# Performance work log

Measured on AMD Instinct MI355X. Metric: run time of the kernel, lower is better.

## Reference

```python
import jax, jax.numpy as jnp
import numpy as np

# dims
B, N, D = 4, 1024, 768
H, HD = 12, 64            # num_heads, head_dim (routed q heads = top-H experts)
EA = 24                   # num_attn_experts
EF, KF = 8, 2             # num_ffd_experts, ffd_heads (top-k for FFN MoE)
HS = int(4 * D) // KF     # ffn expert head_size = 1536
T = 9                     # task_num
S = 1                     # shared FFN experts: max(1, int(8*0.1))


def layernorm(x, g, b, eps=1e-5):
    m = x.mean(-1, keepdims=True)
    v = ((x - m) ** 2).mean(-1, keepdims=True)
    return (x - m) * jax.lax.rsqrt(v + eps) * g + b


def setup_inputs() -> dict:
    key = jax.random.key(0)
    ks = jax.random.split(key, 16)
    s = 0.02
    rn = lambda k, shp: jax.random.normal(k, shp, dtype=jnp.float32)
    return {
        "x": rn(ks[0], (B, N, D)),
        "task_bh": 3,
        "ln1_g": jnp.ones((D,), jnp.float32), "ln1_b": jnp.zeros((D,), jnp.float32),
        "ln2_g": jnp.ones((D,), jnp.float32), "ln2_b": jnp.zeros((D,), jnp.float32),
        "gate_a": rn(ks[1], (T, D, EA)) * s,
        "Wq_in": rn(ks[2], (EA, D, HD)) * s,
        "Wq_out": rn(ks[3], (EA, HD, D)) * s,
        "W_kv": rn(ks[4], (D, 2 * HD)) * s, "b_kv": jnp.zeros((2 * HD,), jnp.float32),
        "gate_f": rn(ks[5], (T, D, EF)) * s,
        "W1f": rn(ks[6], (EF, D, HS)) * s, "b1f": jnp.zeros((EF, HS), jnp.float32),
        "W2f": rn(ks[7], (EF, HS, D)) * s, "b_out": jnp.zeros((D,), jnp.float32),
        "Ws1": rn(ks[8], (S, D, HS)) * s, "bs1": jnp.zeros((S, HS), jnp.float32),
        "Ws2": rn(ks[9], (S, HS, D)) * s,
    }


def _route(h, gate_w, k):
    # h: [B,N,D], gate_w: [D,E] -> normalized top-k weights + one-hot dispatch
    probs = jax.nn.softmax(jnp.einsum("bnd,de->bne", h, gate_w), axis=-1)
    topv, topi = jax.lax.top_k(probs, k)                 # [B,N,k]
    topv = topv / topv.sum(-1, keepdims=True)
    oh = jax.nn.one_hot(topi, probs.shape[-1], dtype=h.dtype)  # [B,N,k,E]
    return topv, oh


def reference(x, task_bh, ln1_g, ln1_b, ln2_g, ln2_b, gate_a, Wq_in, Wq_out,
              W_kv, b_kv, gate_f, W1f, b1f, W2f, b_out, Ws1, bs1, Ws2):
    # --- MoE attention (routed q heads, shared single-head k/v) ---
    h = layernorm(x, ln1_g, ln1_b)
    topv, oh = _route(h, gate_a[task_bh], H)             # [B,N,H], [B,N,H,EA]
    h_all = jnp.einsum("bnd,edh->bneh", h, Wq_in)        # all-expert q projections
    q = jnp.einsum("bnke,bneh->bnkh", oh, h_all)         # gathered q heads [B,N,H,HD]
    kv = h @ W_kv + b_kv
    kk, vv = kv[..., :HD], kv[..., HD:]                  # [B,N,HD]
    att = jnp.einsum("bihd,bjd->bhij", q, kk) * (HD ** -0.5)
    att = jax.nn.softmax(att, axis=-1)
    o = jnp.einsum("bhij,bjd->bihd", att, vv)            # [B,N,H,HD]
    dense = jnp.einsum("bnk,bnke,bnkh->bneh", topv, oh, o)  # scatter to experts
    y = jnp.einsum("bneh,ehd->bnd", dense, Wq_out)       # gated expert output proj
    x = x + y

    # --- MoE FFN (top-KF routed experts + shared experts) ---
    h = layernorm(x, ln2_g, ln2_b)
    topv, oh = _route(h, gate_f[task_bh], KF)            # [B,N,KF], [B,N,KF,EF]
    h_all = jax.nn.gelu(jnp.einsum("bnd,edh->bneh", h, W1f) + b1f, approximate=False)
    wdense = jnp.einsum("bnk,bnke->bne", topv, oh)       # per-expert gate weights
    y = jnp.einsum("bne,bneh,ehd->bnd", wdense, h_all, W2f) + b_out
    hs = jax.nn.gelu(jnp.einsum("bnd,sdh->bnsh", h, Ws1) + bs1, approximate=False)
    y = y + jnp.einsum("bnsh,shd->bnd", hs, Ws2)         # always-on shared experts
    return x + y
```

## Files before the change

kernel.cpp:

```cpp
#include <hip/hip_runtime.h>
#include <hip/hip_bf16.h>

#define NTOK 4096
#define DDIM 768
#define NEA  24
#define NHEAD 12
#define HDIM 64
#define NEF  8
#define HSD  1536
#define SEQL 1024
#define NB   4
#define MAXTILE 104
#define NQKV 1664

using bf16 = __hip_bfloat16;

typedef float v4f __attribute__((ext_vector_type(4)));
typedef short v8s __attribute__((ext_vector_type(8)));
typedef __bf16 v8bf __attribute__((ext_vector_type(8)));

typedef __attribute__((address_space(3))) unsigned lds_u32_t;
typedef const __attribute__((address_space(1))) unsigned glb_u32_t;

__device__ __forceinline__ void gload16(const void* g, void* l) {
  __builtin_amdgcn_global_load_lds((glb_u32_t*)g, (lds_u32_t*)l, 16, 0, 0);
}

__device__ __forceinline__ float gelu_f(float x) {
  return 0.5f * x * (1.0f + erff(x * 0.70710678118654752440f));
}

__device__ __forceinline__ short f2bf_s(float x) {
  bf16 h = __float2bfloat16(x);
  return __builtin_bit_cast(short, h);
}

__device__ __forceinline__ int xcd_swz(int lin, int nwg) {
  return (lin & 7) * (nwg >> 3) + (lin >> 3);
}

__device__ __forceinline__ void gemm_core(const short* gA0, const short* gA1,
                                          const short* gB0, const short* gB1,
                                          short* lA, short* lB, int steps,
                                          v4f (&acc)[4][4])
{
  const int tid = threadIdx.x;
  const int w = tid >> 6, l = tid & 63;
  const int wr = (w >> 1) * 64, wc = (w & 1) * 64;
  const int fr = l & 15, ko = (l >> 4) * 8;
  const int sb = w * 1024;
  gload16(gA0, lA + sb); gload16(gA1, lA + sb + 512);
  gload16(gB0, lB + sb); gload16(gB1, lB + sb + 512);
  gA0 += 32; gA1 += 32; gB0 += 32; gB1 += 32;
  __syncthreads();
  int cur = 0;
  for (int s = 0; s < steps; ++s) {
    const int nxt = cur ^ 1;
    if (s + 1 < steps) {
      gload16(gA0, lA + nxt * 4096 + sb);
      gload16(gA1, lA + nxt * 4096 + sb + 512);
      gload16(gB0, lB + nxt * 4096 + sb);
      gload16(gB1, lB + nxt * 4096 + sb + 512);
      gA0 += 32; gA1 += 32; gB0 += 32; gB1 += 32;
    }
    const short* bA = lA + cur * 4096;
    const short* bB = lB + cur * 4096;
    v8s av[4], bv[4];
#pragma unroll
    for (int mi = 0; mi < 4; ++mi)
      av[mi] = *(const v8s*)(bA + (wr + mi * 16 + fr) * 32 + ko);
#pragma unroll
    for (int ni = 0; ni < 4; ++ni)
      bv[ni] = *(const v8s*)(bB + (wc + ni * 16 + fr) * 32 + ko);
#pragma unroll
    for (int mi = 0; mi < 4; ++mi)
#pragma unroll
      for (int ni = 0; ni < 4; ++ni)
        acc[mi][ni] = __builtin_amdgcn_mfma_f32_16x16x32_bf16(
            __builtin_bit_cast(v8bf, av[mi]), __builtin_bit_cast(v8bf, bv[ni]),
            acc[mi][ni], 0, 0, 0);
    __syncthreads();
    cur = nxt;
  }
}

template<int EPI>
__global__ __launch_bounds__(256, 4) void k_gemm(const short* __restrict__ A,
    const short* __restrict__ Bt, float* __restrict__ C, bf16* __restrict__ Cb,
    const float* __restrict__ addsrc, int N, int K)
{
  const int nwg = gridDim.x * gridDim.y;
  const int swz = xcd_swz(blockIdx.x + gridDim.x * blockIdx.y, nwg);
  const int m0 = (swz % gridDim.x) * 128, n0 = (swz / gridDim.x) * 128;
  __shared__ __align__(16) short lA[2 * 128 * 32];
  __shared__ __align__(16) short lB[2 * 128 * 32];
  const int tid = threadIdx.x, w = tid >> 6, l = tid & 63;
  const int ca = w * 128 + l, cb = ca + 64;
  const short* gA0 = A + (size_t)(m0 + (ca >> 2)) * K + (ca & 3) * 8;
  const short* gA1 = A + (size_t)(m0 + (cb >> 2)) * K + (cb & 3) * 8;
  const short* gB0 = Bt + (size_t)(n0 + (ca >> 2)) * K + (ca & 3) * 8;
  const short* gB1 = Bt + (size_t)(n0 + (cb >> 2)) * K + (cb & 3) * 8;
  v4f acc[4][4];
  v4f z = {0.f, 0.f, 0.f, 0.f};
#pragma unroll
  for (int i = 0; i < 4; ++i)
#pragma unroll
    for (int j = 0; j < 4; ++j) acc[i][j] = z;
  gemm_core(gA0, gA1, gB0, gB1, lA, lB, K >> 5, acc);
  const int wr = (w >> 1) * 64, wc = (w & 1) * 64;
  const int fr = l & 15, rq = (l >> 4) * 4;
#pragma unroll
  for (int mi = 0; mi < 4; ++mi)
#pragma unroll
    for (int ni = 0; ni < 4; ++ni)
#pragma unroll
      for (int j = 0; j < 4; ++j) {
        int rg = m0 + wr + mi * 16 + rq + j;
        int cg = n0 + wc + ni * 16 + fr;
        float v = acc[mi][ni][j];
        if (EPI == 2) v += addsrc[(size_t)rg * N + cg];
        if (EPI == 3) Cb[(size_t)rg * N + cg] = __float2bfloat16(v);
        else          C[(size_t)rg * N + cg] = v;
      }
}

template<int PHASE>
__global__ __launch_bounds__(256, 5) void k_gemm_moe(
    const short* __restrict__ Aact, const short* __restrict__ Wt,
    const short* __restrict__ Wst, const float* __restrict__ b1f,
    const float* __restrict__ bs1, const float* __restrict__ wsl,
    const int* __restrict__ off, const int* __restrict__ cnt,
    const int* __restrict__ list, const int* __restrict__ tmeta,
    const int* __restrict__ ntl, short* __restrict__ outb,
    float* __restrict__ outf)
{
  constexpr int K = (PHASE == 0) ? DDIM : HSD;
  constexpr int N = (PHASE == 0) ? HSD : DDIM;
  const int nwg = gridDim.x * gridDim.y;
  const int swz = xcd_swz(blockIdx.x + gridDim.x * blockIdx.y, nwg);
  const int ti = swz % gridDim.x;
  const int n0 = (swz / gridDim.x) * 128;
  if (ti >= ntl[0]) return;
  const int mm = tmeta[ti];
  const int e = mm >> 20;
  const int r0 = mm & 0xFFFFF;
  const int base = (e < 8) ? off[e] : NTOK * 2;
  const int c    = (e < 8) ? cnt[e] : NTOK;
  const int rows = c - r0;
  const short* Bt = (e < 8) ? Wt + (size_t)e * N * K : Wst;
  __shared__ __align__(16) short lA[2 * 128 * 32];
  __shared__ __align__(16) short lB[2 * 128 * 32];
  const int tid = threadIdx.x, w = tid >> 6, l = tid & 63;
  const int ca = w * 128 + l, cb = ca + 64;

  auto arowptr = [&](int chunk) -> const short* {
    int r = chunk >> 2;
    int re = (r < rows) ? r : (rows - 1);
    int slot = base + r0 + re;
    if (PHASE == 0) {
      int tok = (e < 8) ? list[slot] : (slot - NTOK * 2);
      return Aact + (size_t)tok * DDIM;
    } else {
      return Aact + (size_t)slot * HSD;
    }
  };
  const short* gA0 = arowptr(ca) + (ca & 3) * 8;
  const short* gA1 = arowptr(cb) + (cb & 3) * 8;
  const short* gB0 = Bt + (size_t)(n0 + (ca >> 2)) * K + (ca & 3) * 8;
  const short* gB1 = Bt + (size_t)(n0 + (cb >> 2)) * K + (cb & 3) * 8;
  v4f acc[4][4];
  v4f z = {0.f, 0.f, 0.f, 0.f};
#pragma unroll
  for (int i = 0; i < 4; ++i)
#pragma unroll
    for (int j = 0; j < 4; ++j) acc[i][j] = z;
  gemm_core(gA0, gA1, gB0, gB1, lA, lB, K >> 5, acc);
  const int wr = (w >> 1) * 64, wc = (w & 1) * 64;
  const int fr = l & 15, rq = (l >> 4) * 4;
  const float* bias = (PHASE == 0) ? ((e < 8) ? b1f + e * HSD : bs1) : nullptr;
#pragma unroll
  for (int mi = 0; mi < 4; ++mi)
#pragma unroll
    for (int ni = 0; ni < 4; ++ni)
#pragma unroll
      for (int j = 0; j < 4; ++j) {
        int rl = wr + mi * 16 + rq + j;
        if (rl >= rows) continue;
        int slot = base + r0 + rl;
        int cg = n0 + wc + ni * 16 + fr;
        float v = acc[mi][ni][j];
        if (PHASE == 0) {
          v = gelu_f(v + bias[cg]);
          outb[(size_t)slot * HSD + cg] = f2bf_s(v);
        } else {
          outf[(size_t)slot * DDIM + cg] = v * wsl[slot];
        }
      }
}

__global__ __launch_bounds__(256) void k_lnrouteA(const float* __restrict__ x,
    const float* __restrict__ lg_, const float* __restrict__ lb_,
    const float* __restrict__ gt, bf16* __restrict__ hb,
    int* __restrict__ topi, float* __restrict__ topv)
{
  const int t = blockIdx.x * 4 + (threadIdx.x >> 6);
  const int l = threadIdx.x & 63;
  const float* xr = x + (size_t)t * DDIM;
  float v[12];
  float s = 0.f, q = 0.f;
#pragma unroll
  for (int m = 0; m < 12; ++m) {
    v[m] = xr[l + 64 * m];
    s += v[m]; q += v[m] * v[m];
  }
#pragma unroll
  for (int m = 32; m >= 1; m >>= 1) { s += __shfl_xor(s, m); q += __shfl_xor(q, m); }
  const float mean = s * (1.f / DDIM);
  const float inv = rsqrtf(q * (1.f / DDIM) - mean * mean + 1e-5f);
  float hr[12];
#pragma unroll
  for (int m = 0; m < 12; ++m) {
    int d = l + 64 * m;
    hr[m] = (v[m] - mean) * inv * lg_[d] + lb_[d];
    hb[(size_t)t * DDIM + d] = __float2bfloat16(hr[m]);
  }
  float lg[NEA];
#pragma unroll
  for (int e = 0; e < NEA; ++e) {
    const float* ge = gt + e * DDIM;
    float a = 0.f;
#pragma unroll
    for (int m = 0; m < 12; ++m) a += hr[m] * ge[l + 64 * m];
#pragma unroll
    for (int m = 32; m >= 1; m >>= 1) a += __shfl_xor(a, m);
    lg[e] = a;
  }
  unsigned used = 0;
  int sel[NHEAD]; float bvk[NHEAD];
#pragma unroll
  for (int k = 0; k < NHEAD; ++k) {
    float bv = -3e30f; int best = 0;
#pragma unroll
    for (int e = 0; e < NEA; ++e)
      if (!((used >> e) & 1u) && lg[e] > bv) { bv = lg[e]; best = e; }
    used |= 1u << best; sel[k] = best; bvk[k] = bv;
  }
  const float mx = bvk[0];
  float pvk[NHEAD], ssum = 0.f;
#pragma unroll
  for (int k = 0; k < NHEAD; ++k) { pvk[k] = expf(bvk[k] - mx); ssum += pvk[k]; }
  const float invs = 1.f / ssum;
  if (l == 0) {
#pragma unroll
    for (int k = 0; k < NHEAD; ++k) {
      topi[t * NHEAD + k] = sel[k];
      topv[t * NHEAD + k] = pvk[k] * invs;
    }
  }
}

__global__ __launch_bounds__(256) void k_lnrouteF(const float* __restrict__ x,
    const float* __restrict__ lg_, const float* __restrict__ lb_,
    const float* __restrict__ gt, bf16* __restrict__ hb,
    int* __restrict__ ef, float* __restrict__ wf, int* __restrict__ cnt)
{
  const int t = blockIdx.x * 4 + (threadIdx.x >> 6);
  const int l = threadIdx.x & 63;
  const float* xr = x + (size_t)t * DDIM;
  float v[12];
  float s = 0.f, q = 0.f;
#pragma unroll
  for (int m = 0; m < 12; ++m) {
    v[m] = xr[l + 64 * m];
    s += v[m]; q += v[m] * v[m];
  }
#pragma unroll
  for (int m = 32; m >= 1; m >>= 1) { s += __shfl_xor(s, m); q += __shfl_xor(q, m); }
  const float mean = s * (1.f / DDIM);
  const float inv = rsqrtf(q * (1.f / DDIM) - mean * mean + 1e-5f);
  float hr[12];
#pragma unroll
  for (int m = 0; m < 12; ++m) {
    int d = l + 64 * m;
    hr[m] = (v[m] - mean) * inv * lg_[d] + lb_[d];
    hb[(size_t)t * DDIM + d] = __float2bfloat16(hr[m]);
  }
  float lg[NEF];
#pragma unroll
  for (int e = 0; e < NEF; ++e) {
    const float* ge = gt + e * DDIM;
    float a = 0.f;
#pragma unroll
    for (int m = 0; m < 12; ++m) a += hr[m] * ge[l + 64 * m];
#pragma unroll
    for (int m = 32; m >= 1; m >>= 1) a += __shfl_xor(a, m);
    lg[e] = a;
  }
  unsigned used = 0;
  int sel[2]; float bvk[2];
#pragma unroll
  for (int k = 0; k < 2; ++k) {
    float bv = -3e30f; int best = 0;
#pragma unroll
    for (int e = 0; e < NEF; ++e)
      if (!((used >> e) & 1u) && lg[e] > bv) { bv = lg[e]; best = e; }
    used |= 1u << best; sel[k] = best; bvk[k] = bv;
  }
  const float mx = bvk[0];
  float p0 = expf(bvk[0] - mx), p1 = expf(bvk[1] - mx);
  const float invs = 1.f / (p0 + p1);
  if (l == 0) {
    ef[t * 2 + 0] = sel[0]; wf[t * 2 + 0] = p0 * invs;
    ef[t * 2 + 1] = sel[1]; wf[t * 2 + 1] = p1 * invs;
    atomicAdd(&cnt[sel[0]], 1);
    atomicAdd(&cnt[sel[1]], 1);
  }
}

__global__ void k_packGT(const float* __restrict__ src, const int* __restrict__ task,
                         float* __restrict__ dst, int E)
{
  int idx = blockIdx.x * 256 + threadIdx.x;
  if (idx >= E * DDIM) return;
  int e = idx / DDIM, d = idx - e * DDIM;
  dst[idx] = src[(size_t)task[0] * DDIM * E + (size_t)d * E + e];
}

__global__ void k_off(const int* __restrict__ cnt, int* __restrict__ off,
                      int* __restrict__ cur, int* __restrict__ tmeta,
                      int* __restrict__ ntl)
{
  if (threadIdx.x == 0 && blockIdx.x == 0) {
    int a = 0;
    for (int e = 0; e < NEF; ++e) { off[e] = a; cur[e] = a; a += cnt[e]; }
    off[NEF] = a;
    int n = 0;
    for (int e = 0; e < NEF; ++e)
      for (int r = 0; r < cnt[e]; r += 128) tmeta[n++] = (e << 20) | r;
    for (int r = 0; r < NTOK; r += 128) tmeta[n++] = (8 << 20) | r;
    ntl[0] = n;
  }
}

__global__ void k_fill(const int* __restrict__ ef, const float* __restrict__ wf,
                       int* __restrict__ cur, int* __restrict__ list,
                       float* __restrict__ wsl, int* __restrict__ sof)
{
  int t = blockIdx.x * 256 + threadIdx.x;
  if (t >= NTOK) return;
  for (int k = 0; k < 2; ++k) {
    int e = ef[t * 2 + k];
    int slot = atomicAdd(&cur[e], 1);
    list[slot] = t;
    wsl[slot] = wf[t * 2 + k];
    sof[t * 2 + k] = slot;
  }
  list[NTOK * 2 + t] = t;
  wsl[NTOK * 2 + t] = 1.f;
}

__global__ void k_packKV(const bf16* __restrict__ hq, const float* __restrict__ bkv,
                         bf16* __restrict__ kvb)
{
  int idx = blockIdx.x * 256 + threadIdx.x;
  int t = idx >> 7, j = idx & 127;
  float v = __bfloat162float(hq[(size_t)t * NQKV + 1536 + j]) + bkv[j];
  kvb[idx] = __float2bfloat16(v);
}

__global__ void k_scatter(const float* __restrict__ o, const int* __restrict__ topi,
                          const float* __restrict__ topv, bf16* __restrict__ dense)
{
  int idx = blockIdx.x * 256 + threadIdx.x;
  int t = idx / (NHEAD * HDIM);
  int rem = idx - t * (NHEAD * HDIM);
  int k = rem >> 6, hd = rem & 63;
  float v = topv[t * NHEAD + k] * o[idx];
  dense[(size_t)t * (NEA * HDIM) + topi[t * NHEAD + k] * HDIM + hd] = __float2bfloat16(v);
}

__global__ __launch_bounds__(256, 2) void k_attn_mfma(const bf16* __restrict__ hq,
    const int* __restrict__ topi, const bf16* __restrict__ kv, float* __restrict__ o)
{
  __shared__ __align__(16) short Qs[64 * 64];
  __shared__ __align__(16) short Ks[64 * 64];
  __shared__ __align__(16) short Vs[64 * 64];
  __shared__ __align__(16) short Ps[64 * 64];
  const int i0 = blockIdx.x * 64;
  const int h = blockIdx.y;
  const int b = blockIdx.z;
  const int tid = threadIdx.x;
  const int w = tid >> 6, l = tid & 63;
  const int g = l >> 4, fq = l & 15;
  const short* qg = (const short*)hq;
  const short* kvg = (const short*)kv;

  {
    int c0 = tid, c1 = tid + 256;
    int r0 = c0 >> 3, s0 = (c0 & 7) ^ (r0 & 7);
    int r1 = c1 >> 3, s1 = (c1 & 7) ^ (r1 & 7);
    int t0 = b * SEQL + i0 + r0, t1 = b * SEQL + i0 + r1;
    int e0 = topi[t0 * NHEAD + h], e1 = topi[t1 * NHEAD + h];
    gload16(qg + (size_t)t0 * NQKV + e0 * HDIM + s0 * 8, Qs + w * 512);
    gload16(qg + (size_t)t1 * NQKV + e1 * HDIM + s1 * 8, Qs + 2048 + w * 512);
  }

  float m_run[4], l_run[4];
  v4f oacc[4];
#pragma unroll
  for (int r = 0; r < 4; ++r) { m_run[r] = -1e30f; l_run[r] = 0.f; }
#pragma unroll
  for (int nd = 0; nd < 4; ++nd) oacc[nd] = (v4f){0.f, 0.f, 0.f, 0.f};

  const int vj = tid & 63;
  const int vd0 = (tid >> 6) * 16;

  for (int jt = 0; jt < 16; ++jt) {
    if (jt) __syncthreads();
    {
      int c0 = tid, c1 = tid + 256;
      int r0 = c0 >> 3, s0 = (c0 & 7) ^ (r0 & 7);
      int r1 = c1 >> 3, s1 = (c1 & 7) ^ (r1 & 7);
      gload16(kvg + ((size_t)(b * SEQL + jt * 64 + r0)) * 128 + s0 * 8,
              Ks + w * 512);
      gload16(kvg + ((size_t)(b * SEQL + jt * 64 + r1)) * 128 + s1 * 8,
              Ks + 2048 + w * 512);
    }
    {
      const short* gv = kvg + ((size_t)(b * SEQL + jt * 64 + vj)) * 128 + 64 + vd0;
      v8s a0 = *(const v8s*)gv;
      v8s a1 = *(const v8s*)(gv + 8);
#pragma unroll
      for (int k2 = 0; k2 < 8; ++k2) {
        int d = vd0 + k2;
        Vs[d * 64 + (((vj >> 3) ^ (d & 7)) << 3) + (vj & 7)] = a0[k2];
      }
#pragma unroll
      for (int k2 = 0; k2 < 8; ++k2) {
        int d = vd0 + 8 + k2;
        Vs[d * 64 + (((vj >> 3) ^ (d & 7)) << 3) + (vj & 7)] = a1[k2];
      }
    }
    __syncthreads();

    v8s aq[2];
#pragma unroll
    for (int kk = 0; kk < 2; ++kk)
      aq[kk] = *(const v8s*)&Qs[(16 * w + fq) * 64 + (((kk * 4 + g) ^ (fq & 7)) << 3)];
    v4f sacc[4];
#pragma unroll
    for (int n = 0; n < 4; ++n) {
      sacc[n] = (v4f){0.f, 0.f, 0.f, 0.f};
#pragma unroll
      for (int kk = 0; kk < 2; ++kk) {
        v8s bk = *(const v8s*)&Ks[(16 * n + fq) * 64 + (((kk * 4 + g) ^ (fq & 7)) << 3)];
        sacc[n] = __builtin_amdgcn_mfma_f32_16x16x32_bf16(
            __builtin_bit_cast(v8bf, aq[kk]), __builtin_bit_cast(v8bf, bk),
            sacc[n], 0, 0, 0);
      }
    }
#pragma unroll
    for (int n = 0; n < 4; ++n) sacc[n] *= 0.125f;

#pragma unroll
    for (int r = 0; r < 4; ++r) {
      float mt = fmaxf(fmaxf(sacc[0][r], sacc[1][r]), fmaxf(sacc[2][r], sacc[3][r]));
      mt = fmaxf(mt, __shfl_xor(mt, 1));
      mt = fmaxf(mt, __shfl_xor(mt, 2));
      mt = fmaxf(mt, __shfl_xor(mt, 4));
      mt = fmaxf(mt, __shfl_xor(mt, 8));
      float mnew = fmaxf(m_run[r], mt);
      float corr = __expf(m_run[r] - mnew);
      float pv[4], ps = 0.f;
#pragma unroll
      for (int n = 0; n < 4; ++n) { pv[n] = __expf(sacc[n][r] - mnew); ps += pv[n]; }
      ps += __shfl_xor(ps, 1);
      ps += __shfl_xor(ps, 2);
      ps += __shfl_xor(ps, 4);
      ps += __shfl_xor(ps, 8);
      l_run[r] = l_run[r] * corr + ps;
      m_run[r] = mnew;
#pragma unroll
      for (int nd = 0; nd < 4; ++nd) oacc[nd][r] *= corr;
      int qrow = 16 * w + 4 * g + r;
#pragma unroll
      for (int n = 0; n < 4; ++n)
        Ps[qrow * 64 + (((2 * n + (fq >> 3)) ^ (qrow & 7)) << 3) + (fq & 7)] =
            f2bf_s(pv[n]);
    }
    asm volatile("s_waitcnt lgkmcnt(0)" ::: "memory");
    __builtin_amdgcn_sched_barrier(0);

#pragma unroll
    for (int kk = 0; kk < 2; ++kk) {
      v8s pa = *(const v8s*)&Ps[(16 * w + fq) * 64 + (((kk * 4 + g) ^ (fq & 7)) << 3)];
#pragma unroll
      for (int nd = 0; nd < 4; ++nd) {
        v8s vb = *(const v8s*)&Vs[(16 * nd + fq) * 64 + (((kk * 4 + g) ^ (fq & 7)) << 3)];
        oacc[nd] = __builtin_amdgcn_mfma_f32_16x16x32_bf16(
            __builtin_bit_cast(v8bf, pa), __builtin_bit_cast(v8bf, vb),
            oacc[nd], 0, 0, 0);
      }
    }
  }

#pragma unroll
  for (int r = 0; r < 4; ++r) {
    float inv = 1.f / l_run[r];
    int qgl = i0 + 16 * w + 4 * g + r;
#pragma unroll
    for (int nd = 0; nd < 4; ++nd)
      o[(((size_t)b * SEQL + qgl) * NHEAD + h) * HDIM + 16 * nd + fq] =
          oacc[nd][r] * inv;
  }
}

__global__ __launch_bounds__(256) void k_packT(const float* __restrict__ src,
                                               bf16* __restrict__ dst, int K, int N)
{
  __shared__ float tile[32][33];
  const size_t zoff = (size_t)blockIdx.z * K * N;
  const int k0 = blockIdx.x * 32, n0 = blockIdx.y * 32;
  const int tx = threadIdx.x & 31, ty = threadIdx.x >> 5;
#pragma unroll
  for (int i = 0; i < 32; i += 8)
    tile[ty + i][tx] = src[zoff + (size_t)(k0 + ty + i) * N + n0 + tx];
  __syncthreads();
#pragma unroll
  for (int i = 0; i < 32; i += 8)
    dst[zoff + (size_t)(n0 + ty + i) * K + k0 + tx] =
        __float2bfloat16(tile[tx][ty + i]);
}

__global__ void k_final(const float* __restrict__ x2, const float* __restrict__ bout,
                        const float* __restrict__ yp, const int* __restrict__ sof,
                        float* __restrict__ out)
{
  int idx = blockIdx.x * 256 + threadIdx.x;
  int t = idx / DDIM, d = idx - t * DDIM;
  int s0 = sof[2 * t], s1 = sof[2 * t + 1];
  out[idx] = x2[idx] + bout[d] + yp[(size_t)s0 * DDIM + d] + yp[(size_t)s1 * DDIM + d] +
             yp[((size_t)(NTOK * 2) + t) * DDIM + d];
}

extern "C" void kernel_launch(void* const* d_in, const int* in_sizes, int n_in,
                              void* d_out, int out_size, void* d_ws, size_t ws_size,
                              hipStream_t stream) {
  const float* x      = (const float*)d_in[0];
  const int*   task   = (const int*)d_in[1];
  const float* ln1g   = (const float*)d_in[2];
  const float* ln1b   = (const float*)d_in[3];
  const float* ln2g   = (const float*)d_in[4];
  const float* ln2b   = (const float*)d_in[5];
  const float* gate_a = (const float*)d_in[6];
  const float* wq_in  = (const float*)d_in[7];
  const float* wq_out = (const float*)d_in[8];
  const float* w_kv   = (const float*)d_in[9];
  const float* b_kv   = (const float*)d_in[10];
  const float* gate_f = (const float*)d_in[11];
  const float* w1f    = (const float*)d_in[12];
  const float* b1f    = (const float*)d_in[13];
  const float* w2f    = (const float*)d_in[14];
  const float* b_out  = (const float*)d_in[15];
  const float* ws1    = (const float*)d_in[16];
  const float* bs1    = (const float*)d_in[17];
  const float* ws2    = (const float*)d_in[18];

  char* W = (char*)d_ws;
  size_t off_ = 0;
  auto alloc = [&](size_t b) { size_t o = off_; off_ += (b + 255) & ~(size_t)255; return o; };
  size_t o_reg1  = alloc(37748736);
  size_t o_h1b   = o_reg1;
  size_t o_hallq = o_reg1 + 6291456;
  size_t o_hmid  = o_reg1;
  size_t o_q     = alloc(12582912);
  size_t o_o     = alloc(12582912);
  size_t o_dense = alloc(12582912);
  size_t o_ypart = o_q;
  size_t o_kvb   = alloc(1048576);
  size_t o_x2    = alloc(12582912);
  size_t o_h2b   = alloc(6291456);
  size_t o_btq   = alloc(2555904);
  size_t o_wqot  = alloc(2359296);
  size_t o_w1t   = alloc(18874368);
  size_t o_w2t   = alloc(18874368);
  size_t o_ws1t  = alloc(2359296);
  size_t o_ws2t  = alloc(2359296);
  size_t o_topi  = alloc(196608);
  size_t o_topv  = alloc(196608);
  size_t o_ef    = alloc(32768);
  size_t o_wf    = alloc(32768);
  size_t o_cnt   = alloc(1024);
  size_t o_offs  = alloc(1024);
  size_t o_cur   = alloc(1024);
  size_t o_list  = alloc(49152);
  size_t o_wsl   = alloc(49152);
  size_t o_sof   = alloc(32768);
  size_t o_tmeta = alloc(1024);
  size_t o_ntl   = alloc(256);
  size_t o_gta   = alloc(73728);
  size_t o_gtf   = alloc(24576);
  if (ws_size < off_) return;

  bf16*  h1b   = (bf16*)(W + o_h1b);
  bf16*  hallqb= (bf16*)(W + o_hallq);
  float* ob    = (float*)(W + o_o);
  bf16*  dense = (bf16*)(W + o_dense);
  bf16*  kvbb  = (bf16*)(W + o_kvb);
  float* x2b   = (float*)(W + o_x2);
  bf16*  h2b   = (bf16*)(W + o_h2b);
  short* hmid  = (short*)(W + o_hmid);
  float* ypart = (float*)(W + o_ypart);
  int*   topi  = (int*)(W + o_topi);
  float* topv  = (float*)(W + o_topv);
  int*   efp   = (int*)(W + o_ef);
  float* wfp   = (float*)(W + o_wf);
  int*   cntp  = (int*)(W + o_cnt);
  int*   offp  = (int*)(W + o_offs);
  int*   curp  = (int*)(W + o_cur);
  int*   listp = (int*)(W + o_list);
  float* wslp  = (float*)(W + o_wsl);
  int*   sofp  = (int*)(W + o_sof);
  int*   tmeta = (int*)(W + o_tmeta);
  int*   ntl   = (int*)(W + o_ntl);
  float* gta   = (float*)(W + o_gta);
  float* gtf   = (float*)(W + o_gtf);

  k_packT<<<dim3(24, 2, 24), 256, 0, stream>>>(wq_in, (bf16*)(W + o_btq), 768, 64);
  k_packT<<<dim3(24, 4, 1), 256, 0, stream>>>(w_kv, (bf16*)(W + o_btq) + 1536 * 768, 768, 128);
  k_packT<<<dim3(48, 24, 1), 256, 0, stream>>>(wq_out, (bf16*)(W + o_wqot), 1536, 768);
  k_packT<<<dim3(24, 48, 8), 256, 0, stream>>>(w1f, (bf16*)(W + o_w1t), 768, 1536);
  k_packT<<<dim3(48, 24, 8), 256, 0, stream>>>(w2f, (bf16*)(W + o_w2t), 1536, 768);
  k_packT<<<dim3(24, 48, 1), 256, 0, stream>>>(ws1, (bf16*)(W + o_ws1t), 768, 1536);
  k_packT<<<dim3(48, 24, 1), 256, 0, stream>>>(ws2, (bf16*)(W + o_ws2t), 1536, 768);
  k_packGT<<<dim3(72), 256, 0, stream>>>(gate_a, task, gta, NEA);
  k_packGT<<<dim3(24), 256, 0, stream>>>(gate_f, task, gtf, NEF);

  (void)hipMemsetAsync(W + o_dense, 0, 12582912, stream);
  (void)hipMemsetAsync(W + o_cnt, 0, 64, stream);

  k_lnrouteA<<<NTOK / 4, 256, 0, stream>>>(x, ln1g, ln1b, gta, h1b, topi, topv);

  k_gemm<3><<<dim3(32, 13), 256, 0, stream>>>((const short*)h1b, (const short*)(W + o_btq),
                                              nullptr, hallqb, nullptr, NQKV, 768);

  k_packKV<<<dim3(2048), 256, 0, stream>>>(hallqb, b_kv, kvbb);
  k_attn_mfma<<<dim3(16, NHEAD, NB), 256, 0, stream>>>(hallqb, topi, kvbb, ob);
  k_scatter<<<dim3(12288), 256, 0, stream>>>(ob, topi, topv, dense);

  k_gemm<2><<<dim3(32, 6), 256, 0, stream>>>((const short*)dense, (const short*)(W + o_wqot),
                                             x2b, nullptr, x, 768, 1536);

  k_lnrouteF<<<NTOK / 4, 256, 0, stream>>>(x2b, ln2g, ln2b, gtf, h2b, efp, wfp, cntp);
  k_off<<<1, 1, 0, stream>>>(cntp, offp, curp, tmeta, ntl);
  k_fill<<<16, 256, 0, stream>>>(efp, wfp, curp, listp, wslp, sofp);

  k_gemm_moe<0><<<dim3(MAXTILE, 12), 256, 0, stream>>>((const short*)h2b,
      (const short*)(W + o_w1t), (const short*)(W + o_ws1t), b1f, bs1, nullptr,
      offp, cntp, listp, tmeta, ntl, hmid, nullptr);
  k_gemm_moe<1><<<dim3(MAXTILE, 6), 256, 0, stream>>>((const short*)hmid,
      (const short*)(W + o_w2t), (const short*)(W + o_ws2t), nullptr, nullptr, wslp,
      offp, cntp, listp, tmeta, ntl, nullptr, ypart);

  k_final<<<dim3(12288), 256, 0, stream>>>(x2b, b_out, ypart, sofp, (float*)d_out);
}
```

Baseline: 532.4 us.

## Fuse attention scatter into epilogue, split-K output proj, atomic MoE accumulation

The gated scatter to expert slots moves into the attention epilogue, so the separate scatter kernel and the fp32 attention-output buffer go away. The attention output projection now uses split-K (2 slices) with atomicAdd into a residual buffer prefilled by a device copy of x. The FFN second-phase GEMM atomically accumulates weighted expert outputs per token, so the final kernel no longer gathers slot partials. This trades extra memset/memcpy traffic and atomic contention for fewer kernels and less intermediate memory, and makes the floating-point summation order nondeterministic.

```diff
diff --git a/kernel.cpp b/kernel.cpp
--- a/kernel.cpp
+++ b/kernel.cpp
@@ -87,26 +87,28 @@
 template<int EPI>
 __global__ __launch_bounds__(256, 4) void k_gemm(const short* __restrict__ A,
     const short* __restrict__ Bt, float* __restrict__ C, bf16* __restrict__ Cb,
-    const float* __restrict__ addsrc, int N, int K)
+    int N, int K)
 {
   const int nwg = gridDim.x * gridDim.y;
   const int swz = xcd_swz(blockIdx.x + gridDim.x * blockIdx.y, nwg);
   const int m0 = (swz % gridDim.x) * 128, n0 = (swz / gridDim.x) * 128;
+  const int kspl = (EPI == 4) ? (K / (int)gridDim.z) : K;
+  const int kbase = (EPI == 4) ? (int)blockIdx.z * kspl : 0;
   __shared__ __align__(16) short lA[2 * 128 * 32];
   __shared__ __align__(16) short lB[2 * 128 * 32];
   const int tid = threadIdx.x, w = tid >> 6, l = tid & 63;
   const int ca = w * 128 + l, cb = ca + 64;
-  const short* gA0 = A + (size_t)(m0 + (ca >> 2)) * K + (ca & 3) * 8;
-  const short* gA1 = A + (size_t)(m0 + (cb >> 2)) * K + (cb & 3) * 8;
-  const short* gB0 = Bt + (size_t)(n0 + (ca >> 2)) * K + (ca & 3) * 8;
-  const short* gB1 = Bt + (size_t)(n0 + (cb >> 2)) * K + (cb & 3) * 8;
+  const short* gA0 = A + (size_t)(m0 + (ca >> 2)) * K + (ca & 3) * 8 + kbase;
+  const short* gA1 = A + (size_t)(m0 + (cb >> 2)) * K + (cb & 3) * 8 + kbase;
+  const short* gB0 = Bt + (size_t)(n0 + (ca >> 2)) * K + (ca & 3) * 8 + kbase;
+  const short* gB1 = Bt + (size_t)(n0 + (cb >> 2)) * K + (cb & 3) * 8 + kbase;
   v4f acc[4][4];
   v4f z = {0.f, 0.f, 0.f, 0.f};
 #pragma unroll
   for (int i = 0; i < 4; ++i)
 #pragma unroll
     for (int j = 0; j < 4; ++j) acc[i][j] = z;
-  gemm_core(gA0, gA1, gB0, gB1, lA, lB, K >> 5, acc);
+  gemm_core(gA0, gA1, gB0, gB1, lA, lB, kspl >> 5, acc);
   const int wr = (w >> 1) * 64, wc = (w & 1) * 64;
   const int fr = l & 15, rq = (l >> 4) * 4;
 #pragma unroll
@@ -118,9 +120,9 @@
         int rg = m0 + wr + mi * 16 + rq + j;
         int cg = n0 + wc + ni * 16 + fr;
         float v = acc[mi][ni][j];
-        if (EPI == 2) v += addsrc[(size_t)rg * N + cg];
-        if (EPI == 3) Cb[(size_t)rg * N + cg] = __float2bfloat16(v);
-        else          C[(size_t)rg * N + cg] = v;
+        if (EPI == 3)      Cb[(size_t)rg * N + cg] = __float2bfloat16(v);
+        else if (EPI == 4) atomicAdd(&C[(size_t)rg * N + cg], v);
+        else               C[(size_t)rg * N + cg] = v;
       }
 }
 
@@ -193,7 +195,8 @@
           v = gelu_f(v + bias[cg]);
           outb[(size_t)slot * HSD + cg] = f2bf_s(v);
         } else {
-          outf[(size_t)slot * DDIM + cg] = v * wsl[slot];
+          int tok = (e < 8) ? list[slot] : (slot - NTOK * 2);
+          atomicAdd(&outf[(size_t)tok * DDIM + cg], v * wsl[slot]);
         }
       }
 }
@@ -344,7 +347,7 @@
 
 __global__ void k_fill(const int* __restrict__ ef, const float* __restrict__ wf,
                        int* __restrict__ cur, int* __restrict__ list,
-                       float* __restrict__ wsl, int* __restrict__ sof)
+                       float* __restrict__ wsl)
 {
   int t = blockIdx.x * 256 + threadIdx.x;
   if (t >= NTOK) return;
@@ -353,7 +356,6 @@
     int slot = atomicAdd(&cur[e], 1);
     list[slot] = t;
     wsl[slot] = wf[t * 2 + k];
-    sof[t * 2 + k] = slot;
   }
   list[NTOK * 2 + t] = t;
   wsl[NTOK * 2 + t] = 1.f;
@@ -368,19 +370,9 @@
   kvb[idx] = __float2bfloat16(v);
 }
 
-__global__ void k_scatter(const float* __restrict__ o, const int* __restrict__ topi,
-                          const float* __restrict__ topv, bf16* __restrict__ dense)
-{
-  int idx = blockIdx.x * 256 + threadIdx.x;
-  int t = idx / (NHEAD * HDIM);
-  int rem = idx - t * (NHEAD * HDIM);
-  int k = rem >> 6, hd = rem & 63;
-  float v = topv[t * NHEAD + k] * o[idx];
-  dense[(size_t)t * (NEA * HDIM) + topi[t * NHEAD + k] * HDIM + hd] = __float2bfloat16(v);
-}
-
 __global__ __launch_bounds__(256, 2) void k_attn_mfma(const bf16* __restrict__ hq,
-    const int* __restrict__ topi, const bf16* __restrict__ kv, float* __restrict__ o)
+    const int* __restrict__ topi, const float* __restrict__ topv,
+    const bf16* __restrict__ kv, bf16* __restrict__ dense)
 {
   __shared__ __align__(16) short Qs[64 * 64];
   __shared__ __align__(16) short Ks[64 * 64];
@@ -506,12 +498,13 @@
 
 #pragma unroll
   for (int r = 0; r < 4; ++r) {
-    float inv = 1.f / l_run[r];
-    int qgl = i0 + 16 * w + 4 * g + r;
+    int t = b * SEQL + i0 + 16 * w + 4 * g + r;
+    int e = topi[t * NHEAD + h];
+    float sc = topv[t * NHEAD + h] / l_run[r];
 #pragma unroll
     for (int nd = 0; nd < 4; ++nd)
-      o[(((size_t)b * SEQL + qgl) * NHEAD + h) * HDIM + 16 * nd + fq] =
-          oacc[nd][r] * inv;
+      dense[(size_t)t * (NEA * HDIM) + e * HDIM + 16 * nd + fq] =
+          __float2bfloat16(oacc[nd][r] * sc);
   }
 }
 
@@ -533,14 +526,11 @@
 }
 
 __global__ void k_final(const float* __restrict__ x2, const float* __restrict__ bout,
-                        const float* __restrict__ yp, const int* __restrict__ sof,
-                        float* __restrict__ out)
+                        const float* __restrict__ yacc, float* __restrict__ out)
 {
   int idx = blockIdx.x * 256 + threadIdx.x;
-  int t = idx / DDIM, d = idx - t * DDIM;
-  int s0 = sof[2 * t], s1 = sof[2 * t + 1];
-  out[idx] = x2[idx] + bout[d] + yp[(size_t)s0 * DDIM + d] + yp[(size_t)s1 * DDIM + d] +
-             yp[((size_t)(NTOK * 2) + t) * DDIM + d];
+  int d = idx % DDIM;
+  out[idx] = x2[idx] + bout[d] + yacc[idx];
 }
 
 extern "C" void kernel_launch(void* const* d_in, const int* in_sizes, int n_in,
@@ -573,10 +563,8 @@
   size_t o_h1b   = o_reg1;
   size_t o_hallq = o_reg1 + 6291456;
   size_t o_hmid  = o_reg1;
-  size_t o_q     = alloc(12582912);
-  size_t o_o     = alloc(12582912);
+  size_t o_yacc  = alloc(12582912);
   size_t o_dense = alloc(12582912);
-  size_t o_ypart = o_q;
   size_t o_kvb   = alloc(1048576);
   size_t o_x2    = alloc(12582912);
   size_t o_h2b   = alloc(6291456);
@@ -595,7 +583,6 @@
   size_t o_cur   = alloc(1024);
   size_t o_list  = alloc(49152);
   size_t o_wsl   = alloc(49152);
-  size_t o_sof   = alloc(32768);
   size_t o_tmeta = alloc(1024);
   size_t o_ntl   = alloc(256);
   size_t o_gta   = alloc(73728);
@@ -604,13 +591,12 @@
 
   bf16*  h1b   = (bf16*)(W + o_h1b);
   bf16*  hallqb= (bf16*)(W + o_hallq);
-  float* ob    = (float*)(W + o_o);
+  float* yacc  = (float*)(W + o_yacc);
   bf16*  dense = (bf16*)(W + o_dense);
   bf16*  kvbb  = (bf16*)(W + o_kvb);
   float* x2b   = (float*)(W + o_x2);
   bf16*  h2b   = (bf16*)(W + o_h2b);
   short* hmid  = (short*)(W + o_hmid);
-  float* ypart = (float*)(W + o_ypart);
   int*   topi  = (int*)(W + o_topi);
   float* topv  = (float*)(W + o_topv);
   int*   efp   = (int*)(W + o_ef);
@@ -620,7 +606,6 @@
   int*   curp  = (int*)(W + o_cur);
   int*   listp = (int*)(W + o_list);
   float* wslp  = (float*)(W + o_wsl);
-  int*   sofp  = (int*)(W + o_sof);
   int*   tmeta = (int*)(W + o_tmeta);
   int*   ntl   = (int*)(W + o_ntl);
   float* gta   = (float*)(W + o_gta);
@@ -638,29 +623,31 @@
 
   (void)hipMemsetAsync(W + o_dense, 0, 12582912, stream);
   (void)hipMemsetAsync(W + o_cnt, 0, 64, stream);
+  (void)hipMemsetAsync(W + o_yacc, 0, 12582912, stream);
 
   k_lnrouteA<<<NTOK / 4, 256, 0, stream>>>(x, ln1g, ln1b, gta, h1b, topi, topv);
 
   k_gemm<3><<<dim3(32, 13), 256, 0, stream>>>((const short*)h1b, (const short*)(W + o_btq),
-                                              nullptr, hallqb, nullptr, NQKV, 768);
+                                              nullptr, hallqb, NQKV, 768);
 
   k_packKV<<<dim3(2048), 256, 0, stream>>>(hallqb, b_kv, kvbb);
-  k_attn_mfma<<<dim3(16, NHEAD, NB), 256, 0, stream>>>(hallqb, topi, kvbb, ob);
-  k_scatter<<<dim3(12288), 256, 0, stream>>>(ob, topi, topv, dense);
-
-  k_gemm<2><<<dim3(32, 6), 256, 0, stream>>>((const short*)dense, (const short*)(W + o_wqot),
-                                             x2b, nullptr, x, 768, 1536);
+  k_attn_mfma<<<dim3(16, NHEAD, NB), 256, 0, stream>>>(hallqb, topi, topv, kvbb, dense);
+
+  (void)hipMemcpyAsync(W + o_x2, (const void*)x, 12582912,
+                       hipMemcpyDeviceToDevice, stream);
+  k_gemm<4><<<dim3(32, 6, 2), 256, 0, stream>>>((const short*)dense,
+      (const short*)(W + o_wqot), x2b, nullptr, 768, 1536);
 
   k_lnrouteF<<<NTOK / 4, 256, 0, stream>>>(x2b, ln2g, ln2b, gtf, h2b, efp, wfp, cntp);
   k_off<<<1, 1, 0, stream>>>(cntp, offp, curp, tmeta, ntl);
-  k_fill<<<16, 256, 0, stream>>>(efp, wfp, curp, listp, wslp, sofp);
+  k_fill<<<16, 256, 0, stream>>>(efp, wfp, curp, listp, wslp);
 
   k_gemm_moe<0><<<dim3(MAXTILE, 12), 256, 0, stream>>>((const short*)h2b,
       (const short*)(W + o_w1t), (const short*)(W + o_ws1t), b1f, bs1, nullptr,
       offp, cntp, listp, tmeta, ntl, hmid, nullptr);
   k_gemm_moe<1><<<dim3(MAXTILE, 6), 256, 0, stream>>>((const short*)hmid,
       (const short*)(W + o_w2t), (const short*)(W + o_ws2t), nullptr, nullptr, wslp,
-      offp, cntp, listp, tmeta, ntl, nullptr, ypart);
-
-  k_final<<<dim3(12288), 256, 0, stream>>>(x2b, b_out, ypart, sofp, (float*)d_out);
-}
+      offp, cntp, listp, tmeta, ntl, nullptr, yacc);
+
+  k_final<<<dim3(12288), 256, 0, stream>>>(x2b, b_out, yacc, (float*)d_out);
+}
```

Result: slower. 549.9 us (+3.3%).
